# Kernel tuning notes

Hardware: AMD Instinct MI355X
Metric: run time of the kernel (lower is better)

The kernel has to match this reference:

```python
import jax, jax.numpy as jnp
import numpy as np

EPS = 1e-6
NH, NKV, HD = 16, 8, 256
WIN = 1024
NE, TOPK = 32, 4
H, I = 2816, 704


def _rmsnorm(x, w, eps=EPS):
    x32 = x.astype(jnp.float32)
    n = x32 * jax.lax.rsqrt(jnp.mean(x32 * x32, axis=-1, keepdims=True) + eps)
    return n.astype(x.dtype) * w


def _rotate_half(x):
    x1, x2 = jnp.split(x, 2, axis=-1)
    return jnp.concatenate([-x2, x1], axis=-1)


def setup_inputs() -> dict:
    B, S = 1, 512
    key = jax.random.key(0)
    ks = jax.random.split(key, 10)
    sc = 0.02
    hidden_states = jax.random.normal(ks[0], (B, S, H), jnp.float32)
    # rope tables (sliding_attention: theta=10000, full rotary over head_dim)
    pos = np.arange(S, dtype=np.float64)
    inv = 1.0 / (10000.0 ** (np.arange(0, HD, 2, dtype=np.float64) / HD))
    fr = pos[:, None] * inv[None, :]
    emb = np.concatenate([fr, fr], axis=-1)
    cos = jnp.asarray(np.cos(emb)[None], jnp.float32)
    sin = jnp.asarray(np.sin(emb)[None], jnp.float32)
    return dict(
        hidden_states=hidden_states, cos=cos, sin=sin,
        ln_in_w=jnp.ones((H,), jnp.float32),
        ln_post_attn_w=jnp.ones((H,), jnp.float32),
        ln_pre_ffn_w=jnp.ones((H,), jnp.float32),
        ln_post_ffn_w=jnp.ones((H,), jnp.float32),
        q_w=jax.random.normal(ks[1], (NH * HD, H), jnp.float32) * sc,
        k_w=jax.random.normal(ks[2], (NKV * HD, H), jnp.float32) * sc,
        v_w=jax.random.normal(ks[3], (NKV * HD, H), jnp.float32) * sc,
        o_w=jax.random.normal(ks[4], (H, NH * HD), jnp.float32) * sc,
        q_norm_w=jnp.ones((HD,), jnp.float32),
        k_norm_w=jnp.ones((HD,), jnp.float32),
        router_w=jax.random.normal(ks[5], (NE, H), jnp.float32) * sc,
        router_scale=jnp.ones((H,), jnp.float32),
        w_gate=jax.random.normal(ks[6], (NE, I, H), jnp.float32) * sc,
        w_up=jax.random.normal(ks[7], (NE, I, H), jnp.float32) * sc,
        w_down=jax.random.normal(ks[8], (NE, H, I), jnp.float32) * sc,
    )


def reference(hidden_states, cos, sin, ln_in_w, ln_post_attn_w, ln_pre_ffn_w,
              ln_post_ffn_w, q_w, k_w, v_w, o_w, q_norm_w, k_norm_w,
              router_w, router_scale, w_gate, w_up, w_down):
    B, S, _ = hidden_states.shape
    # ---- attention block ----
    res = hidden_states
    h = _rmsnorm(hidden_states, ln_in_w)
    q = (h @ q_w.T).reshape(B, S, NH, HD)
    k = (h @ k_w.T).reshape(B, S, NKV, HD)
    v = (h @ v_w.T).reshape(B, S, NKV, HD)
    q = _rmsnorm(q, q_norm_w)
    k = _rmsnorm(k, k_norm_w)
    v = _rmsnorm(v, jnp.float32(1.0))  # v_norm has no scale
    c, s = cos[:, :, None, :], sin[:, :, None, :]
    q = q * c + _rotate_half(q) * s
    k = k * c + _rotate_half(k) * s
    kr = jnp.repeat(k, NH // NKV, axis=2)  # GQA expand
    vr = jnp.repeat(v, NH // NKV, axis=2)
    scores = jnp.einsum('bqnd,bknd->bnqk', q, kr)  # softmax scale = 1.0
    ii = jnp.arange(S)[:, None]
    jj = jnp.arange(S)[None, :]
    mask = (jj <= ii) & ((ii - jj) < WIN)  # causal + sliding window
    scores = jnp.where(mask, scores, jnp.finfo(scores.dtype).min)
    attn = jax.nn.softmax(scores, axis=-1)
    o = jnp.einsum('bnqk,bknd->bqnd', attn, vr).reshape(B, S, NH * HD)
    h = _rmsnorm(o @ o_w.T, ln_post_attn_w)
    x = res + h
    # ---- MoE block ----
    res = x
    h = _rmsnorm(x, ln_pre_ffn_w)
    t = h.reshape(B * S, H)
    # router: RMSNorm(no scale) * hidden^-0.5 * scale -> linear -> softmax -> topk
    t32 = t.astype(jnp.float32)
    n = (t32 * jax.lax.rsqrt(jnp.mean(t32 * t32, -1, keepdims=True) + EPS)).astype(t.dtype)
    n = n * (H ** -0.5) * router_scale
    probs = jax.nn.softmax(n @ router_w.T, axis=-1)
    topw, topi = jax.lax.top_k(probs, TOPK)
    topw = topw / jnp.sum(topw, axis=-1, keepdims=True)
    T = t.shape[0]
    combine = jnp.zeros((T, NE), t.dtype).at[jnp.arange(T)[:, None], topi].add(topw)
    # gated MLP per expert (dense eval + sparse combine == torch_moe math)
    g = jnp.einsum('th,eih->eti', t, w_gate)
    u = jnp.einsum('th,eih->eti', t, w_up)
    a = jax.nn.gelu(g, approximate=True) * u
    y = jnp.einsum('eti,ehi->eth', a, w_down)  # [E,T,H]
    moe = jnp.einsum('te,eth->th', combine, y).reshape(B, S, H)
    moe = _rmsnorm(moe, ln_post_ffn_w)
    return res + moe
```

## Files before the change

### kernel.cpp

```cpp
#include <hip/hip_runtime.h>

static constexpr int T_S   = 512;
static constexpr int H_DIM = 2816;
static constexpr int HD_   = 256;
static constexpr int N_E   = 32;
static constexpr int TOPK_ = 4;
static constexpr int I_DIM = 704;
static constexpr int Q_N   = 4096;
static constexpr int KV_N  = 2048;
static constexpr int QKV_N = 8192;
static constexpr int NSLOT = 2048;
static constexpr float EPS_ = 1e-6f;

typedef __attribute__((ext_vector_type(4))) float f32x4;
typedef __attribute__((ext_vector_type(8))) short bf16x8;

static __device__ __forceinline__ ushort f2bf(float f) {
  uint u = __float_as_uint(f);
  u += 0x7fffu + ((u >> 16) & 1u);
  return (ushort)(u >> 16);
}
static __device__ __forceinline__ float bf2f(ushort u) {
  return __uint_as_float((uint)u << 16);
}
static __device__ __forceinline__ void split2(float x, ushort& h, ushort& l2) {
  h = f2bf(x);
  l2 = f2bf(x - bf2f(h));
}
static __device__ __forceinline__ void split8(const float4& a, const float4& b,
                                              uint4& H, uint4& L) {
  ushort h0,l0,h1,l1,h2,l2,h3,l3,h4,l4,h5,l5,h6,l6,h7,l7;
  split2(a.x,h0,l0); split2(a.y,h1,l1); split2(a.z,h2,l2); split2(a.w,h3,l3);
  split2(b.x,h4,l4); split2(b.y,h5,l5); split2(b.z,h6,l6); split2(b.w,h7,l7);
  H = (uint4){ (uint)h0|((uint)h1<<16), (uint)h2|((uint)h3<<16),
               (uint)h4|((uint)h5<<16), (uint)h6|((uint)h7<<16) };
  L = (uint4){ (uint)l0|((uint)l1<<16), (uint)l2|((uint)l3<<16),
               (uint)l4|((uint)l5<<16), (uint)l6|((uint)l7<<16) };
}
static __device__ __forceinline__ uint4 pack8(const float4& a, const float4& b) {
  return (uint4){ (uint)f2bf(a.x)|((uint)f2bf(a.y)<<16), (uint)f2bf(a.z)|((uint)f2bf(a.w)<<16),
                  (uint)f2bf(b.x)|((uint)f2bf(b.y)<<16), (uint)f2bf(b.z)|((uint)f2bf(b.w)<<16) };
}

static __device__ __forceinline__ float wave_sum(float v) {
  #pragma unroll
  for (int off = 1; off < 64; off <<= 1) v += __shfl_xor(v, off);
  return v;
}
static __device__ __forceinline__ float block_sum256(float v, float* sm) {
  v = wave_sum(v);
  int w = threadIdx.x >> 6, l = threadIdx.x & 63;
  if (l == 0) sm[w] = v;
  __syncthreads();
  float r = sm[0] + sm[1] + sm[2] + sm[3];
  __syncthreads();
  return r;
}

__global__ __launch_bounds__(256) void k_ln_in(
    const float* __restrict__ hid, const float* __restrict__ w,
    ushort* __restrict__ hhi, ushort* __restrict__ hlo) {
  __shared__ float sm[4];
  int t = blockIdx.x, tid = threadIdx.x;
  const float* row = hid + (size_t)t * H_DIM;
  float x[11]; float s = 0.f;
  #pragma unroll
  for (int j = 0; j < 11; ++j) { x[j] = row[tid + j*256]; s += x[j]*x[j]; }
  s = block_sum256(s, sm);
  float r = rsqrtf(s / (float)H_DIM + EPS_);
  #pragma unroll
  for (int j = 0; j < 11; ++j) {
    int idx = tid + j*256;
    float val = x[j]*r*w[idx];
    ushort h, l2; split2(val, h, l2);
    hhi[(size_t)t*H_DIM + idx] = h;
    hlo[(size_t)t*H_DIM + idx] = l2;
  }
}

__global__ __launch_bounds__(256, 2) void k_gemm_qkv(
    const ushort* __restrict__ Ah, const ushort* __restrict__ Al,
    const float* __restrict__ qw, const float* __restrict__ kw,
    const float* __restrict__ vw, float* __restrict__ Cp) {
  const int K = H_DIM, KS = H_DIM/2, NSs = KS/32;
  __shared__ ushort Ash[4][129][8], Asl[4][129][8];
  __shared__ ushort Bsh[4][65][8],  Bsl[4][65][8];
  int tid = threadIdx.x, w = tid >> 6, l = tid & 63;
  int n0 = blockIdx.x * 64, m0 = blockIdx.y * 128, kz = blockIdx.z;
  int kbase = kz * KS;
  const float* Bp = (n0 < Q_N) ? qw + (size_t)n0*K
                  : (n0 < Q_N+KV_N) ? kw + (size_t)(n0-Q_N)*K
                  : vw + (size_t)(n0-Q_N-KV_N)*K;
  float* C = Cp + (size_t)kz * T_S * QKV_N;
  const int l15 = l & 15, lq = l >> 4;
  const int wm = w >> 1, wn = w & 1;
  const int sar = tid >> 2, sak = tid & 3;
  const ushort* aph = Ah + (size_t)(m0 + sar)*K + kbase + sak*8;
  const ushort* apl = Al + (size_t)(m0 + sar)*K + kbase + sak*8;
  const float*  bp  = Bp + (size_t)sar*K + kbase + sak*8;
  uint4 arh0 = *(const uint4*)(aph);
  uint4 arh1 = *(const uint4*)(aph + (size_t)64*K);
  uint4 arl0 = *(const uint4*)(apl);
  uint4 arl1 = *(const uint4*)(apl + (size_t)64*K);
  float4 brA = *(const float4*)(bp), brB = *(const float4*)(bp + 4);
  f32x4 acc[4][2];
  #pragma unroll
  for (int a = 0; a < 4; ++a)
    #pragma unroll
    for (int b = 0; b < 2; ++b) acc[a][b] = (f32x4){0.f,0.f,0.f,0.f};
  for (int t = 0; t < NSs; ++t) {
    *(uint4*)&Ash[sak][sar][0]    = arh0;
    *(uint4*)&Ash[sak][64+sar][0] = arh1;
    *(uint4*)&Asl[sak][sar][0]    = arl0;
    *(uint4*)&Asl[sak][64+sar][0] = arl1;
    { uint4 H, L; split8(brA, brB, H, L);
      *(uint4*)&Bsh[sak][sar][0] = H;
      *(uint4*)&Bsl[sak][sar][0] = L; }
    __syncthreads();
    if (t + 1 < NSs) {
      int k0 = (t+1)*32;
      arh0 = *(const uint4*)(aph + k0);
      arh1 = *(const uint4*)(aph + (size_t)64*K + k0);
      arl0 = *(const uint4*)(apl + k0);
      arl1 = *(const uint4*)(apl + (size_t)64*K + k0);
      brA = *(const float4*)(bp + k0); brB = *(const float4*)(bp + k0 + 4);
    }
    bf16x8 bh[2], bl[2];
    #pragma unroll
    for (int nf = 0; nf < 2; ++nf) {
      bh[nf] = *(bf16x8*)&Bsh[lq][wn*32 + nf*16 + l15][0];
      bl[nf] = *(bf16x8*)&Bsl[lq][wn*32 + nf*16 + l15][0];
    }
    #pragma unroll
    for (int mf = 0; mf < 4; ++mf) {
// ... 293 lines not shown
    float* __restrict__ topw, int* __restrict__ counts, int* __restrict__ lists) {
  __shared__ float sm[4];
  __shared__ float nrow[H_DIM];
  __shared__ float lg[N_E];
  int t = blockIdx.x, tid = threadIdx.x;
  float ap[11], hd[11]; float s = 0.f;
  #pragma unroll
  for (int j = 0; j < 11; ++j) {
    int idx = tid + j*256;
    ap[j] = aproj0[(size_t)t*H_DIM + idx] + aproj1[(size_t)t*H_DIM + idx];
    hd[j] = hid[(size_t)t*H_DIM + idx];
    s += ap[j]*ap[j];
  }
  s = block_sum256(s, sm);
  float r1 = rsqrtf(s / (float)H_DIM + EPS_);
  float x[11]; float s2 = 0.f;
  #pragma unroll
  for (int j = 0; j < 11; ++j) {
    int idx = tid + j*256;
    x[j] = hd[j] + ap[j]*r1*w_pa[idx];
    s2 += x[j]*x[j];
    xout[(size_t)t*H_DIM + idx] = x[j];
  }
  s2 = block_sum256(s2, sm);
  float r2 = rsqrtf(s2 / (float)H_DIM + EPS_);
  float tv[11]; float s3 = 0.f;
  #pragma unroll
  for (int j = 0; j < 11; ++j) {
    int idx = tid + j*256;
    tv[j] = x[j]*r2*w_pf[idx];
    s3 += tv[j]*tv[j];
    tbf[(size_t)t*H_DIM + idx] = f2bf(tv[j]);
  }
  s3 = block_sum256(s3, sm);
  float r3 = rsqrtf(s3 / (float)H_DIM + EPS_) * rsqrtf((float)H_DIM);
  #pragma unroll
  for (int j = 0; j < 11; ++j) {
    int idx = tid + j*256;
    nrow[idx] = tv[j]*r3*rscale[idx];
  }
  __syncthreads();
  int w = tid >> 6, l = tid & 63;
  #pragma unroll
  for (int ei = 0; ei < 8; ++ei) {
    int e = w*8 + ei;
    const float* rwp = rw + (size_t)e*H_DIM;
    float p = 0.f;
    #pragma unroll 4
    for (int j = 0; j < 44; ++j) p += nrow[l + j*64] * rwp[l + j*64];
    p = wave_sum(p);
    if (l == 0) lg[e] = p;
  }
  __syncthreads();
  if (w == 0) {
    float le = (l < 32) ? lg[l] : -3e38f;
    float m = le;
    #pragma unroll
    for (int off = 1; off < 64; off <<= 1) m = fmaxf(m, __shfl_xor(m, off));
    float p = (l < 32) ? __expf(le - m) : -2.f;
    float v = p; int vi = (l < 32) ? l : 999;
    float selv[TOPK_]; int seli[TOPK_];
    for (int sx = 0; sx < TOPK_; ++sx) {
      float bv = v; int bi = vi;
      #pragma unroll
      for (int off = 1; off < 64; off <<= 1) {
        float ov = __shfl_xor(bv, off); int oi = __shfl_xor(bi, off);
        if (ov > bv || (ov == bv && oi < bi)) { bv = ov; bi = oi; }
      }
      selv[sx] = bv; seli[sx] = bi;
      if (vi == bi) v = -1.f;
    }
    if (l == 0) {
      float wsum = selv[0]+selv[1]+selv[2]+selv[3];
      for (int sx = 0; sx < TOPK_; ++sx) {
        topw[t*TOPK_ + sx] = selv[sx]/wsum;
        int e = seli[sx];
        int pos = atomicAdd(&counts[e], 1);
        lists[e*T_S + pos] = t*TOPK_ + sx;
      }
    }
  }
}

__global__ __launch_bounds__(256, 2) void k_moe_gateup(
    const ushort* __restrict__ tbf, const float* __restrict__ wg,
    const float* __restrict__ wu, const int* __restrict__ counts,
    const int* __restrict__ lists, float* __restrict__ pg, float* __restrict__ pu) {
  const int K = H_DIM, KS = K/4, NS = KS/32;
  __shared__ ushort As[4][129][8];
  __shared__ ushort Bg[4][65][8], Bu[4][65][8];
  __shared__ int lls[128];
  int tid = threadIdx.x, w = tid >> 6, l = tid & 63;
  int e = blockIdx.y, n0 = blockIdx.x * 64;
  int mz = blockIdx.z >> 2, kz = blockIdx.z & 3;
  int m0 = mz * 128, kbase = kz * KS;
  int ne = counts[e];
  if (m0 >= ne) return;
  const int* list = lists + e*T_S;
  if (tid < 128) lls[tid] = (m0 + tid < ne) ? list[m0 + tid] : list[0];
  __syncthreads();
  const int l15 = l & 15, lq = l >> 4;
  const int wm = w >> 1, wn = w & 1;
  const int arow = tid >> 1, aoct = (tid & 1) * 2;
  const ushort* ap = tbf + (size_t)(lls[arow] >> 2)*K + kbase + aoct*8;
  const int bhalf = tid >> 7, brow = (tid & 127) >> 1, boct = (tid & 1) * 2;
  const float* bp = (bhalf ? wu : wg) + ((size_t)e*I_DIM + n0 + brow)*K + kbase + boct*8;
  uint4 a0 = *(const uint4*)(ap), a1 = *(const uint4*)(ap + 8);
  float4 b0 = *(const float4*)(bp),     b1 = *(const float4*)(bp + 4);
  float4 b2 = *(const float4*)(bp + 8), b3 = *(const float4*)(bp + 12);
  f32x4 ag[4][2], au[4][2];
  #pragma unroll
  for (int a = 0; a < 4; ++a)
    #pragma unroll
    for (int b = 0; b < 2; ++b) { ag[a][b] = (f32x4){0.f,0.f,0.f,0.f}; au[a][b] = (f32x4){0.f,0.f,0.f,0.f}; }
  for (int t = 0; t < NS; ++t) {
    *(uint4*)&As[aoct][arow][0]   = a0;
    *(uint4*)&As[aoct+1][arow][0] = a1;
    if (bhalf == 0) {
      *(uint4*)&Bg[boct][brow][0]   = pack8(b0, b1);
      *(uint4*)&Bg[boct+1][brow][0] = pack8(b2, b3);
    } else {
      *(uint4*)&Bu[boct][brow][0]   = pack8(b0, b1);
      *(uint4*)&Bu[boct+1][brow][0] = pack8(b2, b3);
    }
    __syncthreads();
    if (t + 1 < NS) {
      int k0 = (t+1)*32;
      a0 = *(const uint4*)(ap + k0); a1 = *(const uint4*)(ap + k0 + 8);
      b0 = *(const float4*)(bp + k0);     b1 = *(const float4*)(bp + k0 + 4);
      b2 = *(const float4*)(bp + k0 + 8); b3 = *(const float4*)(bp + k0 + 12);
    }
    bf16x8 bgf[2], buf_[2];
    #pragma unroll
    for (int nf = 0; nf < 2; ++nf) {
      bgf[nf]  = *(bf16x8*)&Bg[lq][wn*32 + nf*16 + l15][0];
      buf_[nf] = *(bf16x8*)&Bu[lq][wn*32 + nf*16 + l15][0];
    }
    #pragma unroll
    for (int mf = 0; mf < 4; ++mf) {
      bf16x8 af = *(bf16x8*)&As[lq][wm*64 + mf*16 + l15][0];
      #pragma unroll
      for (int nf = 0; nf < 2; ++nf) {
        ag[mf][nf] = __builtin_amdgcn_mfma_f32_16x16x32_bf16(af, bgf[nf],  ag[mf][nf], 0, 0, 0);
        au[mf][nf] = __builtin_amdgcn_mfma_f32_16x16x32_bf16(af, buf_[nf], au[mf][nf], 0, 0, 0);
      }
    }
    __syncthreads();
  }
  const size_t PSL = (size_t)NSLOT * I_DIM;
  #pragma unroll
  for (int mf = 0; mf < 4; ++mf)
    #pragma unroll
    for (int r = 0; r < 4; ++r) {
      int row = wm*64 + mf*16 + lq*4 + r;
      if (m0 + row < ne) {
        size_t base = (size_t)kz*PSL + (size_t)lls[row]*I_DIM + n0 + wn*32;
        #pragma unroll
        for (int nf = 0; nf < 2; ++nf) {
          pg[base + nf*16 + l15] = ag[mf][nf][r];
          pu[base + nf*16 + l15] = au[mf][nf][r];
        }
      }
    }
}

__global__ __launch_bounds__(192) void k_gelu_reduce(
    const float* __restrict__ pg, const float* __restrict__ pu,
    ushort* __restrict__ abf) {
  int sidx = blockIdx.x, c = threadIdx.x;
  if (c >= 176) return;
  const size_t S4 = (size_t)NSLOT * I_DIM / 4;
  const float4* g = (const float4*)(pg + (size_t)sidx*I_DIM) + c;
  const float4* u = (const float4*)(pu + (size_t)sidx*I_DIM) + c;
  float4 gs = g[0], us = u[0];
  #pragma unroll
  for (int k = 1; k < 4; ++k) {
    float4 gk = g[k*S4], uk = u[k*S4];
    gs.x += gk.x; gs.y += gk.y; gs.z += gk.z; gs.w += gk.w;
    us.x += uk.x; us.y += uk.y; us.z += uk.z; us.w += uk.w;
  }
  float go[4] = {gs.x, gs.y, gs.z, gs.w}, uo[4] = {us.x, us.y, us.z, us.w};
  ushort o[4];
  #pragma unroll
  for (int i = 0; i < 4; ++i) {
    float gg = go[i];
    float th = tanhf(0.7978845608f*(gg + 0.044715f*gg*gg*gg));
    o[i] = f2bf(0.5f*gg*(1.f + th)*uo[i]);
  }
  *(ushort4*)(abf + (size_t)sidx*I_DIM + c*4) = *(ushort4*)o;
}

__global__ __launch_bounds__(256, 2) void k_moe_down(
    const ushort* __restrict__ abf, const float* __restrict__ wd,
    const int* __restrict__ counts, const int* __restrict__ lists,
    float* __restrict__ yp) {
  const int K = I_DIM, KS = K/2, NS = KS/32;
  __shared__ ushort As[4][129][8];
  __shared__ ushort Bs[4][129][8];
  __shared__ int lls[128];
  int tid = threadIdx.x, w = tid >> 6, l = tid & 63;
  int e = blockIdx.y, n0 = blockIdx.x * 128;
  int mz = blockIdx.z >> 1, kz = blockIdx.z & 1;
  int m0 = mz * 128, kbase = kz * KS;
  int ne = counts[e];
  if (m0 >= ne) return;
  const int* list = lists + e*T_S;
  if (tid < 128) lls[tid] = (m0 + tid < ne) ? list[m0 + tid] : 0;
  __syncthreads();
  const int l15 = l & 15, lq = l >> 4;
  const int wm = w >> 1, wn = w & 1;
  const int arow = tid >> 1, aoct = (tid & 1) * 2;
  const ushort* ap = abf + (size_t)lls[arow]*K + kbase + aoct*8;
  const int brow = tid >> 1, boct = (tid & 1) * 2;
  const float* bp = wd + ((size_t)e*H_DIM + n0 + brow)*K + kbase + boct*8;
  uint4 a0 = *(const uint4*)(ap), a1 = *(const uint4*)(ap + 8);
  float4 b0 = *(const float4*)(bp),     b1 = *(const float4*)(bp + 4);
  float4 b2 = *(const float4*)(bp + 8), b3 = *(const float4*)(bp + 12);
  f32x4 acc[4][4];
  #pragma unroll
  for (int a = 0; a < 4; ++a)
    #pragma unroll
    for (int b = 0; b < 4; ++b) acc[a][b] = (f32x4){0.f,0.f,0.f,0.f};
  for (int t = 0; t < NS; ++t) {
    *(uint4*)&As[aoct][arow][0]   = a0;
    *(uint4*)&As[aoct+1][arow][0] = a1;
    *(uint4*)&Bs[boct][brow][0]   = pack8(b0, b1);
    *(uint4*)&Bs[boct+1][brow][0] = pack8(b2, b3);
    __syncthreads();
    if (t + 1 < NS) {
      int k0 = (t+1)*32;
      a0 = *(const uint4*)(ap + k0); a1 = *(const uint4*)(ap + k0 + 8);
      b0 = *(const float4*)(bp + k0);     b1 = *(const float4*)(bp + k0 + 4);
      b2 = *(const float4*)(bp + k0 + 8); b3 = *(const float4*)(bp + k0 + 12);
    }
    bf16x8 bf[4];
    #pragma unroll
    for (int nf = 0; nf < 4; ++nf)
      bf[nf] = *(bf16x8*)&Bs[lq][wn*64 + nf*16 + l15][0];
    #pragma unroll
    for (int mf = 0; mf < 4; ++mf) {
      bf16x8 af = *(bf16x8*)&As[lq][wm*64 + mf*16 + l15][0];
      #pragma unroll
      for (int nf = 0; nf < 4; ++nf)
        acc[mf][nf] = __builtin_amdgcn_mfma_f32_16x16x32_bf16(af, bf[nf], acc[mf][nf], 0, 0, 0);
    }
    __syncthreads();
  }
  const size_t YSL = (size_t)NSLOT * H_DIM;
  #pragma unroll
  for (int mf = 0; mf < 4; ++mf)
    #pragma unroll
    for (int r = 0; r < 4; ++r) {
      int row = wm*64 + mf*16 + lq*4 + r;
      if (m0 + row < ne) {
        size_t base = (size_t)kz*YSL + (size_t)lls[row]*H_DIM + n0 + wn*64;
        #pragma unroll
        for (int nf = 0; nf < 4; ++nf)
          yp[base + nf*16 + l15] = acc[mf][nf][r];
      }
    }
}

__global__ __launch_bounds__(256) void k_combine(
    const float* __restrict__ yp, const float* __restrict__ topw,
    const float* __restrict__ xin, const float* __restrict__ w_pff,
    float* __restrict__ out) {
  __shared__ float sm[4];
  const size_t YSL = (size_t)NSLOT * H_DIM;
  int t = blockIdx.x, tid = threadIdx.x;
  float w0 = topw[t*4+0], w1 = topw[t*4+1], w2 = topw[t*4+2], w3 = topw[t*4+3];
  const float* y0 = yp + (size_t)(t*4+0)*H_DIM;
  const float* y1 = yp + (size_t)(t*4+1)*H_DIM;
  const float* y2 = yp + (size_t)(t*4+2)*H_DIM;
  const float* y3 = yp + (size_t)(t*4+3)*H_DIM;
  float m[11]; float s = 0.f;
  #pragma unroll
  for (int j = 0; j < 11; ++j) {
    int idx = tid + j*256;
    m[j] = w0*(y0[idx]+y0[YSL+idx]) + w1*(y1[idx]+y1[YSL+idx])
         + w2*(y2[idx]+y2[YSL+idx]) + w3*(y3[idx]+y3[YSL+idx]);
    s += m[j]*m[j];
  }
  s = block_sum256(s, sm);
  float r = rsqrtf(s / (float)H_DIM + EPS_);
  #pragma unroll
  for (int j = 0; j < 11; ++j) {
    int idx = tid + j*256;
    out[(size_t)t*H_DIM + idx] = xin[(size_t)t*H_DIM + idx] + m[j]*r*w_pff[idx];
  }
}

extern "C" void kernel_launch(void* const* d_in, const int* in_sizes, int n_in,
                              void* d_out, int out_size, void* d_ws, size_t ws_size,
                              hipStream_t stream) {
  (void)in_sizes; (void)n_in; (void)out_size; (void)ws_size;
  const float* hid   = (const float*)d_in[0];
  const float* cosb  = (const float*)d_in[1];
  const float* sinb  = (const float*)d_in[2];
  const float* w_in  = (const float*)d_in[3];
  const float* w_pa  = (const float*)d_in[4];
  const float* w_pf  = (const float*)d_in[5];
  const float* w_pff = (const float*)d_in[6];
  const float* qw    = (const float*)d_in[7];
  const float* kw    = (const float*)d_in[8];
  const float* vw    = (const float*)d_in[9];
  const float* ow    = (const float*)d_in[10];
  const float* qnw   = (const float*)d_in[11];
  const float* knw   = (const float*)d_in[12];
  const float* rw    = (const float*)d_in[13];
  const float* rsc   = (const float*)d_in[14];
  const float* wg    = (const float*)d_in[15];
  const float* wu    = (const float*)d_in[16];
  const float* wd    = (const float*)d_in[17];

  char* ws = (char*)d_ws;
  size_t off = 0;
  auto alloc = [&](size_t sz) { size_t o = off; off += (sz + 255) & ~(size_t)255; return o; };
  size_t oR1  = alloc(46137344);
  size_t ohh  = alloc((size_t)T_S*H_DIM*2);
  size_t ohl  = alloc((size_t)T_S*H_DIM*2);
  size_t oqh  = alloc((size_t)T_S*QKV_N*2);
  size_t oql  = alloc((size_t)T_S*QKV_N*2);
  size_t ovh  = alloc((size_t)8*HD_*T_S*2);
  size_t ovl  = alloc((size_t)8*HD_*T_S*2);
  size_t ox   = alloc((size_t)T_S*H_DIM*4);
  size_t otbf = alloc((size_t)T_S*H_DIM*2);
  size_t otw  = alloc((size_t)T_S*TOPK_*4);
  size_t ocnt = alloc((size_t)N_E*4);
  size_t olst = alloc((size_t)N_E*T_S*4);

  const size_t APRJ_SLICE = (size_t)T_S * H_DIM * 4;

  float*  qkvf0 = (float*)(ws + oR1);
  float*  qkvf1 = (float*)(ws + oR1 + 16777216);
  ushort* o_hi  = (ushort*)(ws + oR1);
  ushort* o_lo  = (ushort*)(ws + oR1 + 4194304);
  float*  aprj0 = (float*)(ws + oR1 + 8388608);
  float*  aprj1 = (float*)(ws + oR1 + 8388608 + APRJ_SLICE);
  float*  pg    = (float*)(ws + oR1);
  float*  pu    = (float*)(ws + oR1 + 23068672);
  float*  yp    = (float*)(ws + oR1);
  ushort* abf   = (ushort*)(ws + ohh);

  k_ln_in<<<dim3(T_S), dim3(256), 0, stream>>>(hid, w_in, (ushort*)(ws+ohh), (ushort*)(ws+ohl));
  k_gemm_qkv<<<dim3(128, 4, 2), dim3(256), 0, stream>>>((ushort*)(ws+ohh), (ushort*)(ws+ohl),
                                                        qw, kw, vw, qkvf0);
  k_norm_rope<<<dim3(T_S*32), dim3(64), 0, stream>>>(qkvf0, qkvf1, cosb, sinb, qnw, knw,
                                                     (ushort*)(ws+oqh), (ushort*)(ws+oql),
                                                     (ushort*)(ws+ovh), (ushort*)(ws+ovl));
  k_attn<<<dim3(8, 16), dim3(256), 0, stream>>>((ushort*)(ws+oqh), (ushort*)(ws+oql),
                                                (ushort*)(ws+ovh), (ushort*)(ws+ovl), o_hi, o_lo);
  k_gemm_oproj<<<dim3(44, 4, 2), dim3(256), 0, stream>>>(o_hi, o_lo, ow, aprj0);
  k_zero_counts<<<dim3(1), dim3(64), 0, stream>>>((int*)(ws+ocnt));
  k_fuse_router<<<dim3(T_S), dim3(256), 0, stream>>>(hid, aprj0, aprj1, w_pa, w_pf, rsc, rw,
                                                     (float*)(ws+ox), (ushort*)(ws+otbf),
                                                     (float*)(ws+otw), (int*)(ws+ocnt), (int*)(ws+olst));
  k_moe_gateup<<<dim3(11, N_E, 16), dim3(256), 0, stream>>>((ushort*)(ws+otbf), wg, wu,
                                                            (int*)(ws+ocnt), (int*)(ws+olst), pg, pu);
  k_gelu_reduce<<<dim3(NSLOT), dim3(192), 0, stream>>>(pg, pu, abf);
  k_moe_down<<<dim3(22, N_E, 8), dim3(256), 0, stream>>>(abf, wd,
                                                         (int*)(ws+ocnt), (int*)(ws+olst), yp);
  k_combine<<<dim3(T_S), dim3(256), 0, stream>>>(yp, (float*)(ws+otw), (float*)(ws+ox),
                                                 w_pff, (float*)d_out);
}
```

Before: 610.9 us.

## Restructure MoE GEMMs to stream weights directly and loop over token tiles

Both MoE expert GEMMs now stage the whole K-slice of gathered activations for a 64-token tile in shared memory. Each wave streams its fp32 weight columns straight from global into registers, with no shared-memory staging for B. Each block loops over all of its expert's token tiles, so weights are read once per (expert, column, k-split) instead of once per 128-token tile. Gate/up now uses an 8-way K split with bf16 partial outputs to cut partial-buffer traffic, at some cost in reduction precision, and down uses a 2-way split. The risks are lower parallelism when experts get many tokens, exposed global-load latency without a prefetch pipeline, and bf16 rounding of the partial sums.

```diff
diff --git a/kernel.cpp b/kernel.cpp
--- a/kernel.cpp
+++ b/kernel.cpp
@@ -509,183 +509,160 @@
   }
 }
 
-__global__ __launch_bounds__(256, 2) void k_moe_gateup(
+__global__ __launch_bounds__(256, 3) void k_moe_gateup(
     const ushort* __restrict__ tbf, const float* __restrict__ wg,
     const float* __restrict__ wu, const int* __restrict__ counts,
-    const int* __restrict__ lists, float* __restrict__ pg, float* __restrict__ pu) {
-  const int K = H_DIM, KS = K/4, NS = KS/32;
-  __shared__ ushort As[4][129][8];
-  __shared__ ushort Bg[4][65][8], Bu[4][65][8];
-  __shared__ int lls[128];
+    const int* __restrict__ lists, ushort* __restrict__ pgb, ushort* __restrict__ pub) {
+  const int K = H_DIM, KS = K/8, NSTEP = KS/32;
+  __shared__ ushort As[44][67][8];
+  __shared__ int lls[64];
   int tid = threadIdx.x, w = tid >> 6, l = tid & 63;
-  int e = blockIdx.y, n0 = blockIdx.x * 64;
-  int mz = blockIdx.z >> 2, kz = blockIdx.z & 3;
-  int m0 = mz * 128, kbase = kz * KS;
+  int e = blockIdx.y, n0 = blockIdx.x * 64, kz = blockIdx.z;
+  int kbase = kz * KS;
   int ne = counts[e];
-  if (m0 >= ne) return;
   const int* list = lists + e*T_S;
-  if (tid < 128) lls[tid] = (m0 + tid < ne) ? list[m0 + tid] : list[0];
-  __syncthreads();
   const int l15 = l & 15, lq = l >> 4;
-  const int wm = w >> 1, wn = w & 1;
-  const int arow = tid >> 1, aoct = (tid & 1) * 2;
-  const ushort* ap = tbf + (size_t)(lls[arow] >> 2)*K + kbase + aoct*8;
-  const int bhalf = tid >> 7, brow = (tid & 127) >> 1, boct = (tid & 1) * 2;
-  const float* bp = (bhalf ? wu : wg) + ((size_t)e*I_DIM + n0 + brow)*K + kbase + boct*8;
-  uint4 a0 = *(const uint4*)(ap), a1 = *(const uint4*)(ap + 8);
-  float4 b0 = *(const float4*)(bp),     b1 = *(const float4*)(bp + 4);
-  float4 b2 = *(const float4*)(bp + 8), b3 = *(const float4*)(bp + 12);
-  f32x4 ag[4][2], au[4][2];
-  #pragma unroll
-  for (int a = 0; a < 4; ++a)
-    #pragma unroll
-    for (int b = 0; b < 2; ++b) { ag[a][b] = (f32x4){0.f,0.f,0.f,0.f}; au[a][b] = (f32x4){0.f,0.f,0.f,0.f}; }
-  for (int t = 0; t < NS; ++t) {
-    *(uint4*)&As[aoct][arow][0]   = a0;
-    *(uint4*)&As[aoct+1][arow][0] = a1;
-    if (bhalf == 0) {
-      *(uint4*)&Bg[boct][brow][0]   = pack8(b0, b1);
-      *(uint4*)&Bg[boct+1][brow][0] = pack8(b2, b3);
-    } else {
-      *(uint4*)&Bu[boct][brow][0]   = pack8(b0, b1);
-      *(uint4*)&Bu[boct+1][brow][0] = pack8(b2, b3);
-    }
-    __syncthreads();
-    if (t + 1 < NS) {
-      int k0 = (t+1)*32;
-      a0 = *(const uint4*)(ap + k0); a1 = *(const uint4*)(ap + k0 + 8);
-      b0 = *(const float4*)(bp + k0);     b1 = *(const float4*)(bp + k0 + 4);
-      b2 = *(const float4*)(bp + k0 + 8); b3 = *(const float4*)(bp + k0 + 12);
-    }
-    bf16x8 bgf[2], buf_[2];
-    #pragma unroll
-    for (int nf = 0; nf < 2; ++nf) {
-      bgf[nf]  = *(bf16x8*)&Bg[lq][wn*32 + nf*16 + l15][0];
-      buf_[nf] = *(bf16x8*)&Bu[lq][wn*32 + nf*16 + l15][0];
-    }
-    #pragma unroll
-    for (int mf = 0; mf < 4; ++mf) {
-      bf16x8 af = *(bf16x8*)&As[lq][wm*64 + mf*16 + l15][0];
-      #pragma unroll
-      for (int nf = 0; nf < 2; ++nf) {
-        ag[mf][nf] = __builtin_amdgcn_mfma_f32_16x16x32_bf16(af, bgf[nf],  ag[mf][nf], 0, 0, 0);
-        au[mf][nf] = __builtin_amdgcn_mfma_f32_16x16x32_bf16(af, buf_[nf], au[mf][nf], 0, 0, 0);
-      }
-    }
-    __syncthreads();
-  }
+  const float* Bmat = (w < 2) ? wg : wu;
+  ushort* Pout = (w < 2) ? pgb : pub;
+  const int col0 = n0 + (w & 1) * 32;
+  const float* bptr0 = Bmat + ((size_t)e*I_DIM + col0 + l15)*K + kbase + lq*8;
+  const float* bptr1 = Bmat + ((size_t)e*I_DIM + col0 + 16 + l15)*K + kbase + lq*8;
   const size_t PSL = (size_t)NSLOT * I_DIM;
-  #pragma unroll
-  for (int mf = 0; mf < 4; ++mf)
-    #pragma unroll
-    for (int r = 0; r < 4; ++r) {
-      int row = wm*64 + mf*16 + lq*4 + r;
-      if (m0 + row < ne) {
-        size_t base = (size_t)kz*PSL + (size_t)lls[row]*I_DIM + n0 + wn*32;
-        #pragma unroll
-        for (int nf = 0; nf < 2; ++nf) {
-          pg[base + nf*16 + l15] = ag[mf][nf][r];
-          pu[base + nf*16 + l15] = au[mf][nf][r];
+  for (int m0 = 0; m0 < ne; m0 += 64) {
+    if (m0 > 0) __syncthreads();
+    if (tid < 64) lls[tid] = (m0 + tid < ne) ? list[m0 + tid] : list[0];
+    __syncthreads();
+    #pragma unroll
+    for (int p = 0; p < 11; ++p) {
+      int c = p*256 + tid;
+      int row = c / 44, oct = c - row*44;
+      const ushort* src = tbf + (size_t)(lls[row] >> 2)*K + kbase + oct*8;
+      *(uint4*)&As[oct][row][0] = *(const uint4*)src;
+    }
+    __syncthreads();
+    f32x4 acc[4][2];
+    #pragma unroll
+    for (int a = 0; a < 4; ++a)
+      #pragma unroll
+      for (int b = 0; b < 2; ++b) acc[a][b] = (f32x4){0.f,0.f,0.f,0.f};
+    for (int s = 0; s < NSTEP; ++s) {
+      int k0 = s*32;
+      float4 f00 = *(const float4*)(bptr0 + k0);
+      float4 f01 = *(const float4*)(bptr0 + k0 + 4);
+      float4 f10 = *(const float4*)(bptr1 + k0);
+      float4 f11 = *(const float4*)(bptr1 + k0 + 4);
+      uint4 B0 = pack8(f00, f01), B1 = pack8(f10, f11);
+      bf16x8 b0 = *(bf16x8*)&B0, b1 = *(bf16x8*)&B1;
+      int ko = s*4 + lq;
+      #pragma unroll
+      for (int mf = 0; mf < 4; ++mf) {
+        bf16x8 af = *(bf16x8*)&As[ko][mf*16 + l15][0];
+        acc[mf][0] = __builtin_amdgcn_mfma_f32_16x16x32_bf16(af, b0, acc[mf][0], 0, 0, 0);
+        acc[mf][1] = __builtin_amdgcn_mfma_f32_16x16x32_bf16(af, b1, acc[mf][1], 0, 0, 0);
+      }
+    }
+    #pragma unroll
+    for (int mf = 0; mf < 4; ++mf)
+      #pragma unroll
+      for (int r = 0; r < 4; ++r) {
+        int row = mf*16 + lq*4 + r;
+        if (m0 + row < ne) {
+          size_t base = (size_t)kz*PSL + (size_t)lls[row]*I_DIM + col0;
+          Pout[base + l15]      = f2bf(acc[mf][0][r]);
+          Pout[base + 16 + l15] = f2bf(acc[mf][1][r]);
         }
       }
-    }
+  }
 }
 
 __global__ __launch_bounds__(192) void k_gelu_reduce(
-    const float* __restrict__ pg, const float* __restrict__ pu,
+    const ushort* __restrict__ pgb, const ushort* __restrict__ pub,
     ushort* __restrict__ abf) {
   int sidx = blockIdx.x, c = threadIdx.x;
   if (c >= 176) return;
-  const size_t S4 = (size_t)NSLOT * I_DIM / 4;
-  const float4* g = (const float4*)(pg + (size_t)sidx*I_DIM) + c;
-  const float4* u = (const float4*)(pu + (size_t)sidx*I_DIM) + c;
-  float4 gs = g[0], us = u[0];
-  #pragma unroll
-  for (int k = 1; k < 4; ++k) {
-    float4 gk = g[k*S4], uk = u[k*S4];
-    gs.x += gk.x; gs.y += gk.y; gs.z += gk.z; gs.w += gk.w;
-    us.x += uk.x; us.y += uk.y; us.z += uk.z; us.w += uk.w;
-  }
-  float go[4] = {gs.x, gs.y, gs.z, gs.w}, uo[4] = {us.x, us.y, us.z, us.w};
+  const size_t S8 = (size_t)NSLOT * I_DIM;
+  const ushort* g = pgb + (size_t)sidx*I_DIM + c*4;
+  const ushort* u = pub + (size_t)sidx*I_DIM + c*4;
+  float gs[4] = {0.f,0.f,0.f,0.f}, us[4] = {0.f,0.f,0.f,0.f};
+  #pragma unroll
+  for (int k = 0; k < 8; ++k) {
+    ushort4 gv = *(const ushort4*)(g + k*S8);
+    ushort4 uv = *(const ushort4*)(u + k*S8);
+    gs[0] += bf2f(gv.x); gs[1] += bf2f(gv.y); gs[2] += bf2f(gv.z); gs[3] += bf2f(gv.w);
+    us[0] += bf2f(uv.x); us[1] += bf2f(uv.y); us[2] += bf2f(uv.z); us[3] += bf2f(uv.w);
+  }
   ushort o[4];
   #pragma unroll
   for (int i = 0; i < 4; ++i) {
-    float gg = go[i];
+    float gg = gs[i];
     float th = tanhf(0.7978845608f*(gg + 0.044715f*gg*gg*gg));
-    o[i] = f2bf(0.5f*gg*(1.f + th)*uo[i]);
+    o[i] = f2bf(0.5f*gg*(1.f + th)*us[i]);
   }
   *(ushort4*)(abf + (size_t)sidx*I_DIM + c*4) = *(ushort4*)o;
 }
 
-__global__ __launch_bounds__(256, 2) void k_moe_down(
+__global__ __launch_bounds__(256, 3) void k_moe_down(
     const ushort* __restrict__ abf, const float* __restrict__ wd,
     const int* __restrict__ counts, const int* __restrict__ lists,
     float* __restrict__ yp) {
-  const int K = I_DIM, KS = K/2, NS = KS/32;
-  __shared__ ushort As[4][129][8];
-  __shared__ ushort Bs[4][129][8];
-  __shared__ int lls[128];
+  const int K = I_DIM, KS = K/2, NSTEP = KS/32;
+  __shared__ ushort As[44][67][8];
+  __shared__ int lls[64];
   int tid = threadIdx.x, w = tid >> 6, l = tid & 63;
-  int e = blockIdx.y, n0 = blockIdx.x * 128;
-  int mz = blockIdx.z >> 1, kz = blockIdx.z & 1;
-  int m0 = mz * 128, kbase = kz * KS;
+  int e = blockIdx.y, n0 = blockIdx.x * 128, kz = blockIdx.z;
+  int kbase = kz * KS;
   int ne = counts[e];
-  if (m0 >= ne) return;
   const int* list = lists + e*T_S;
-  if (tid < 128) lls[tid] = (m0 + tid < ne) ? list[m0 + tid] : 0;
-  __syncthreads();
   const int l15 = l & 15, lq = l >> 4;
-  const int wm = w >> 1, wn = w & 1;
-  const int arow = tid >> 1, aoct = (tid & 1) * 2;
-  const ushort* ap = abf + (size_t)lls[arow]*K + kbase + aoct*8;
-  const int brow = tid >> 1, boct = (tid & 1) * 2;
-  const float* bp = wd + ((size_t)e*H_DIM + n0 + brow)*K + kbase + boct*8;
-  uint4 a0 = *(const uint4*)(ap), a1 = *(const uint4*)(ap + 8);
-  float4 b0 = *(const float4*)(bp),     b1 = *(const float4*)(bp + 4);
-  float4 b2 = *(const float4*)(bp + 8), b3 = *(const float4*)(bp + 12);
-  f32x4 acc[4][4];
-  #pragma unroll
-  for (int a = 0; a < 4; ++a)
-    #pragma unroll
-    for (int b = 0; b < 4; ++b) acc[a][b] = (f32x4){0.f,0.f,0.f,0.f};
-  for (int t = 0; t < NS; ++t) {
-    *(uint4*)&As[aoct][arow][0]   = a0;
-    *(uint4*)&As[aoct+1][arow][0] = a1;
-    *(uint4*)&Bs[boct][brow][0]   = pack8(b0, b1);
-    *(uint4*)&Bs[boct+1][brow][0] = pack8(b2, b3);
-    __syncthreads();
-    if (t + 1 < NS) {
-      int k0 = (t+1)*32;
-      a0 = *(const uint4*)(ap + k0); a1 = *(const uint4*)(ap + k0 + 8);
-      b0 = *(const float4*)(bp + k0);     b1 = *(const float4*)(bp + k0 + 4);
-      b2 = *(const float4*)(bp + k0 + 8); b3 = *(const float4*)(bp + k0 + 12);
-    }
-    bf16x8 bf[4];
-    #pragma unroll
-    for (int nf = 0; nf < 4; ++nf)
-      bf[nf] = *(bf16x8*)&Bs[lq][wn*64 + nf*16 + l15][0];
-    #pragma unroll
-    for (int mf = 0; mf < 4; ++mf) {
-      bf16x8 af = *(bf16x8*)&As[lq][wm*64 + mf*16 + l15][0];
-      #pragma unroll
-      for (int nf = 0; nf < 4; ++nf)
-        acc[mf][nf] = __builtin_amdgcn_mfma_f32_16x16x32_bf16(af, bf[nf], acc[mf][nf], 0, 0, 0);
-    }
-    __syncthreads();
-  }
+  const int col0 = n0 + w * 32;
+  const float* bptr0 = wd + ((size_t)e*H_DIM + col0 + l15)*K + kbase + lq*8;
+  const float* bptr1 = wd + ((size_t)e*H_DIM + col0 + 16 + l15)*K + kbase + lq*8;
   const size_t YSL = (size_t)NSLOT * H_DIM;
-  #pragma unroll
-  for (int mf = 0; mf < 4; ++mf)
-    #pragma unroll
-    for (int r = 0; r < 4; ++r) {
-      int row = wm*64 + mf*16 + lq*4 + r;
-      if (m0 + row < ne) {
-        size_t base = (size_t)kz*YSL + (size_t)lls[row]*H_DIM + n0 + wn*64;
-        #pragma unroll
-        for (int nf = 0; nf < 4; ++nf)
-          yp[base + nf*16 + l15] = acc[mf][nf][r];
-      }
-    }
+  for (int m0 = 0; m0 < ne; m0 += 64) {
+    if (m0 > 0) __syncthreads();
+    if (tid < 64) lls[tid] = (m0 + tid < ne) ? list[m0 + tid] : 0;
+    __syncthreads();
+    #pragma unroll
+    for (int p = 0; p < 11; ++p) {
+      int c = p*256 + tid;
+      int row = c / 44, oct = c - row*44;
+      const ushort* src = abf + (size_t)lls[row]*K + kbase + oct*8;
+      *(uint4*)&As[oct][row][0] = *(const uint4*)src;
+    }
+    __syncthreads();
+    f32x4 acc[4][2];
+    #pragma unroll
+    for (int a = 0; a < 4; ++a)
+      #pragma unroll
+      for (int b = 0; b < 2; ++b) acc[a][b] = (f32x4){0.f,0.f,0.f,0.f};
+    for (int s = 0; s < NSTEP; ++s) {
+      int k0 = s*32;
+      float4 f00 = *(const float4*)(bptr0 + k0);
+      float4 f01 = *(const float4*)(bptr0 + k0 + 4);
+      float4 f10 = *(const float4*)(bptr1 + k0);
+      float4 f11 = *(const float4*)(bptr1 + k0 + 4);
+      uint4 B0 = pack8(f00, f01), B1 = pack8(f10, f11);
+      bf16x8 b0 = *(bf16x8*)&B0, b1 = *(bf16x8*)&B1;
+      int ko = s*4 + lq;
+      #pragma unroll
+      for (int mf = 0; mf < 4; ++mf) {
+        bf16x8 af = *(bf16x8*)&As[ko][mf*16 + l15][0];
+        acc[mf][0] = __builtin_amdgcn_mfma_f32_16x16x32_bf16(af, b0, acc[mf][0], 0, 0, 0);
+        acc[mf][1] = __builtin_amdgcn_mfma_f32_16x16x32_bf16(af, b1, acc[mf][1], 0, 0, 0);
+      }
+    }
+    #pragma unroll
+    for (int mf = 0; mf < 4; ++mf)
+      #pragma unroll
+      for (int r = 0; r < 4; ++r) {
+        int row = mf*16 + lq*4 + r;
+        if (m0 + row < ne) {
+          size_t base = (size_t)kz*YSL + (size_t)lls[row]*H_DIM + col0;
+          yp[base + l15]      = acc[mf][0][r];
+          yp[base + 16 + l15] = acc[mf][1][r];
+        }
+      }
+  }
 }
 
 __global__ __launch_bounds__(256) void k_combine(
@@ -764,8 +741,8 @@
   ushort* o_lo  = (ushort*)(ws + oR1 + 4194304);
   float*  aprj0 = (float*)(ws + oR1 + 8388608);
   float*  aprj1 = (float*)(ws + oR1 + 8388608 + APRJ_SLICE);
-  float*  pg    = (float*)(ws + oR1);
-  float*  pu    = (float*)(ws + oR1 + 23068672);
+  ushort* pgb   = (ushort*)(ws + oR1);
+  ushort* pub   = (ushort*)(ws + oR1 + 23068672);
   float*  yp    = (float*)(ws + oR1);
   ushort* abf   = (ushort*)(ws + ohh);
 
@@ -782,10 +759,10 @@
   k_fuse_router<<<dim3(T_S), dim3(256), 0, stream>>>(hid, aprj0, aprj1, w_pa, w_pf, rsc, rw,
                                                      (float*)(ws+ox), (ushort*)(ws+otbf),
                                                      (float*)(ws+otw), (int*)(ws+ocnt), (int*)(ws+olst));
-  k_moe_gateup<<<dim3(11, N_E, 16), dim3(256), 0, stream>>>((ushort*)(ws+otbf), wg, wu,
-                                                            (int*)(ws+ocnt), (int*)(ws+olst), pg, pu);
-  k_gelu_reduce<<<dim3(NSLOT), dim3(192), 0, stream>>>(pg, pu, abf);
-  k_moe_down<<<dim3(22, N_E, 8), dim3(256), 0, stream>>>(abf, wd,
+  k_moe_gateup<<<dim3(11, N_E, 8), dim3(256), 0, stream>>>((ushort*)(ws+otbf), wg, wu,
+                                                           (int*)(ws+ocnt), (int*)(ws+olst), pgb, pub);
+  k_gelu_reduce<<<dim3(NSLOT), dim3(192), 0, stream>>>(pgb, pub, abf);
+  k_moe_down<<<dim3(22, N_E, 2), dim3(256), 0, stream>>>(abf, wd,
                                                          (int*)(ws+ocnt), (int*)(ws+olst), yp);
   k_combine<<<dim3(T_S), dim3(256), 0, stream>>>(yp, (float*)(ws+otw), (float*)(ws+ox),
                                                  w_pff, (float*)d_out);
```

Result: slower. 656.4 us (+7.4%).

## Stage MoE GEMM tiles via direct global-to-LDS loads and raise occupancy

Applied to the files above, without the earlier changes.

The MoE gate/up and down GEMM kernels now copy A and fp32 B tiles straight from global memory into LDS with global_load_lds, replacing the register-staged loads, and convert B to bf16 when reading it out of LDS. Launch bounds go from 2 to 4 blocks per SM, since fewer registers are held for prefetched tiles. The register double-buffered prefetch is gone, so loads are no longer overlapped with MFMA work except through the extra resident blocks. The fp32 B tile doubles its LDS footprint, and the padded layouts were dropped, which may add bank conflicts.

```diff
diff --git a/kernel.cpp b/kernel.cpp
--- a/kernel.cpp
+++ b/kernel.cpp
@@ -41,6 +41,14 @@
   return (uint4){ (uint)f2bf(a.x)|((uint)f2bf(a.y)<<16), (uint)f2bf(a.z)|((uint)f2bf(a.w)<<16),
                   (uint)f2bf(b.x)|((uint)f2bf(b.y)<<16), (uint)f2bf(b.z)|((uint)f2bf(b.w)<<16) };
 }
+static __device__ __forceinline__ ushort4 pack4(const float4& a) {
+  return (ushort4){ f2bf(a.x), f2bf(a.y), f2bf(a.z), f2bf(a.w) };
+}
+static __device__ __forceinline__ void gld_lds16(const void* g, void* l) {
+  __builtin_amdgcn_global_load_lds(
+      (const __attribute__((address_space(1))) uint*)g,
+      (__attribute__((address_space(3))) uint*)l, 16, 0, 0);
+}
 
 static __device__ __forceinline__ float wave_sum(float v) {
   #pragma unroll
@@ -48,8 +56,8 @@
   return v;
 }
 static __device__ __forceinline__ float block_sum256(float v, float* sm) {
+  int w = threadIdx.x >> 6, l = threadIdx.x & 63;
   v = wave_sum(v);
-  int w = threadIdx.x >> 6, l = threadIdx.x & 63;
   if (l == 0) sm[w] = v;
   __syncthreads();
   float r = sm[0] + sm[1] + sm[2] + sm[3];
@@ -509,13 +517,14 @@
   }
 }
 
-__global__ __launch_bounds__(256, 2) void k_moe_gateup(
+__global__ __launch_bounds__(256, 4) void k_moe_gateup(
     const ushort* __restrict__ tbf, const float* __restrict__ wg,
     const float* __restrict__ wu, const int* __restrict__ counts,
     const int* __restrict__ lists, float* __restrict__ pg, float* __restrict__ pu) {
   const int K = H_DIM, KS = K/4, NS = KS/32;
-  __shared__ ushort As[4][129][8];
-  __shared__ ushort Bg[4][65][8], Bu[4][65][8];
+  __shared__ ushort As[4][128][8];
+  __shared__ float  Bg[8][64][4];
+  __shared__ float  Bu[8][64][4];
   __shared__ int lls[128];
   int tid = threadIdx.x, w = tid >> 6, l = tid & 63;
   int e = blockIdx.y, n0 = blockIdx.x * 64;
@@ -528,40 +537,45 @@
   __syncthreads();
   const int l15 = l & 15, lq = l >> 4;
   const int wm = w >> 1, wn = w & 1;
-  const int arow = tid >> 1, aoct = (tid & 1) * 2;
-  const ushort* ap = tbf + (size_t)(lls[arow] >> 2)*K + kbase + aoct*8;
-  const int bhalf = tid >> 7, brow = (tid & 127) >> 1, boct = (tid & 1) * 2;
-  const float* bp = (bhalf ? wu : wg) + ((size_t)e*I_DIM + n0 + brow)*K + kbase + boct*8;
-  uint4 a0 = *(const uint4*)(ap), a1 = *(const uint4*)(ap + 8);
-  float4 b0 = *(const float4*)(bp),     b1 = *(const float4*)(bp + 4);
-  float4 b2 = *(const float4*)(bp + 8), b3 = *(const float4*)(bp + 12);
+  int cA0 = (w*2+0)*64 + l, cA1 = (w*2+1)*64 + l;
+  const ushort* gA0 = tbf + (size_t)(lls[cA0 & 127] >> 2)*K + kbase + (cA0 >> 7)*8;
+  const ushort* gA1 = tbf + (size_t)(lls[cA1 & 127] >> 2)*K + kbase + (cA1 >> 7)*8;
+  const float* gG0 = wg + ((size_t)e*I_DIM + n0 + (cA0 & 63))*K + kbase + (cA0 >> 6)*4;
+  const float* gG1 = wg + ((size_t)e*I_DIM + n0 + (cA1 & 63))*K + kbase + (cA1 >> 6)*4;
+  const float* gU0 = wu + ((size_t)e*I_DIM + n0 + (cA0 & 63))*K + kbase + (cA0 >> 6)*4;
+  const float* gU1 = wu + ((size_t)e*I_DIM + n0 + (cA1 & 63))*K + kbase + (cA1 >> 6)*4;
+  char* lA0 = (char*)As + (w*2+0)*1024;
+  char* lA1 = (char*)As + (w*2+1)*1024;
+  char* lG0 = (char*)Bg + (w*2+0)*1024;
+  char* lG1 = (char*)Bg + (w*2+1)*1024;
+  char* lU0 = (char*)Bu + (w*2+0)*1024;
+  char* lU1 = (char*)Bu + (w*2+1)*1024;
   f32x4 ag[4][2], au[4][2];
   #pragma unroll
   for (int a = 0; a < 4; ++a)
     #pragma unroll
     for (int b = 0; b < 2; ++b) { ag[a][b] = (f32x4){0.f,0.f,0.f,0.f}; au[a][b] = (f32x4){0.f,0.f,0.f,0.f}; }
   for (int t = 0; t < NS; ++t) {
-    *(uint4*)&As[aoct][arow][0]   = a0;
-    *(uint4*)&As[aoct+1][arow][0] = a1;
-    if (bhalf == 0) {
-      *(uint4*)&Bg[boct][brow][0]   = pack8(b0, b1);
-      *(uint4*)&Bg[boct+1][brow][0] = pack8(b2, b3);
-    } else {
-      *(uint4*)&Bu[boct][brow][0]   = pack8(b0, b1);
-      *(uint4*)&Bu[boct+1][brow][0] = pack8(b2, b3);
-    }
-    __syncthreads();
-    if (t + 1 < NS) {
-      int k0 = (t+1)*32;
-      a0 = *(const uint4*)(ap + k0); a1 = *(const uint4*)(ap + k0 + 8);
-      b0 = *(const float4*)(bp + k0);     b1 = *(const float4*)(bp + k0 + 4);
-      b2 = *(const float4*)(bp + k0 + 8); b3 = *(const float4*)(bp + k0 + 12);
-    }
+    int ko = t*32;
+    __syncthreads();
+    gld_lds16(gA0 + ko, lA0);
+    gld_lds16(gA1 + ko, lA1);
+    gld_lds16(gG0 + ko, lG0);
+    gld_lds16(gG1 + ko, lG1);
+    gld_lds16(gU0 + ko, lU0);
+    gld_lds16(gU1 + ko, lU1);
+    __syncthreads();
     bf16x8 bgf[2], buf_[2];
     #pragma unroll
     for (int nf = 0; nf < 2; ++nf) {
-      bgf[nf]  = *(bf16x8*)&Bg[lq][wn*32 + nf*16 + l15][0];
-      buf_[nf] = *(bf16x8*)&Bu[lq][wn*32 + nf*16 + l15][0];
+      int rowb = wn*32 + nf*16 + l15;
+      float4 g0 = *(const float4*)&Bg[lq*2+0][rowb][0];
+      float4 g1 = *(const float4*)&Bg[lq*2+1][rowb][0];
+      float4 u0 = *(const float4*)&Bu[lq*2+0][rowb][0];
+      float4 u1 = *(const float4*)&Bu[lq*2+1][rowb][0];
+      uint4 G = pack8(g0, g1), U = pack8(u0, u1);
+      bgf[nf] = *(bf16x8*)&G;
+      buf_[nf] = *(bf16x8*)&U;
     }
     #pragma unroll
     for (int mf = 0; mf < 4; ++mf) {
@@ -572,7 +586,6 @@
         au[mf][nf] = __builtin_amdgcn_mfma_f32_16x16x32_bf16(af, buf_[nf], au[mf][nf], 0, 0, 0);
       }
     }
-    __syncthreads();
   }
   const size_t PSL = (size_t)NSLOT * I_DIM;
   #pragma unroll
@@ -617,13 +630,13 @@
   *(ushort4*)(abf + (size_t)sidx*I_DIM + c*4) = *(ushort4*)o;
 }
 
-__global__ __launch_bounds__(256, 2) void k_moe_down(
+__global__ __launch_bounds__(256, 4) void k_moe_down(
     const ushort* __restrict__ abf, const float* __restrict__ wd,
     const int* __restrict__ counts, const int* __restrict__ lists,
     float* __restrict__ yp) {
   const int K = I_DIM, KS = K/2, NS = KS/32;
-  __shared__ ushort As[4][129][8];
-  __shared__ ushort Bs[4][129][8];
+  __shared__ ushort As[4][128][8];
+  __shared__ float  Bs[8][128][4];
   __shared__ int lls[128];
   int tid = threadIdx.x, w = tid >> 6, l = tid & 63;
   int e = blockIdx.y, n0 = blockIdx.x * 128;
@@ -636,34 +649,44 @@
   __syncthreads();
   const int l15 = l & 15, lq = l >> 4;
   const int wm = w >> 1, wn = w & 1;
-  const int arow = tid >> 1, aoct = (tid & 1) * 2;
-  const ushort* ap = abf + (size_t)lls[arow]*K + kbase + aoct*8;
-  const int brow = tid >> 1, boct = (tid & 1) * 2;
-  const float* bp = wd + ((size_t)e*H_DIM + n0 + brow)*K + kbase + boct*8;
-  uint4 a0 = *(const uint4*)(ap), a1 = *(const uint4*)(ap + 8);
-  float4 b0 = *(const float4*)(bp),     b1 = *(const float4*)(bp + 4);
-  float4 b2 = *(const float4*)(bp + 8), b3 = *(const float4*)(bp + 12);
+  int cA0 = (w*2+0)*64 + l, cA1 = (w*2+1)*64 + l;
+  const ushort* gA0 = abf + (size_t)lls[cA0 & 127]*K + kbase + (cA0 >> 7)*8;
+  const ushort* gA1 = abf + (size_t)lls[cA1 & 127]*K + kbase + (cA1 >> 7)*8;
+  int cB0 = (w*4+0)*64 + l, cB1 = (w*4+1)*64 + l, cB2 = (w*4+2)*64 + l, cB3 = (w*4+3)*64 + l;
+  const float* gB0 = wd + ((size_t)e*H_DIM + n0 + (cB0 & 127))*K + kbase + (cB0 >> 7)*4;
+  const float* gB1 = wd + ((size_t)e*H_DIM + n0 + (cB1 & 127))*K + kbase + (cB1 >> 7)*4;
+  const float* gB2 = wd + ((size_t)e*H_DIM + n0 + (cB2 & 127))*K + kbase + (cB2 >> 7)*4;
+  const float* gB3 = wd + ((size_t)e*H_DIM + n0 + (cB3 & 127))*K + kbase + (cB3 >> 7)*4;
+  char* lA0 = (char*)As + (w*2+0)*1024;
+  char* lA1 = (char*)As + (w*2+1)*1024;
+  char* lB0 = (char*)Bs + (w*4+0)*1024;
+  char* lB1 = (char*)Bs + (w*4+1)*1024;
+  char* lB2 = (char*)Bs + (w*4+2)*1024;
+  char* lB3 = (char*)Bs + (w*4+3)*1024;
   f32x4 acc[4][4];
   #pragma unroll
   for (int a = 0; a < 4; ++a)
     #pragma unroll
     for (int b = 0; b < 4; ++b) acc[a][b] = (f32x4){0.f,0.f,0.f,0.f};
   for (int t = 0; t < NS; ++t) {
-    *(uint4*)&As[aoct][arow][0]   = a0;
-    *(uint4*)&As[aoct+1][arow][0] = a1;
-    *(uint4*)&Bs[boct][brow][0]   = pack8(b0, b1);
-    *(uint4*)&Bs[boct+1][brow][0] = pack8(b2, b3);
-    __syncthreads();
-    if (t + 1 < NS) {
-      int k0 = (t+1)*32;
-      a0 = *(const uint4*)(ap + k0); a1 = *(const uint4*)(ap + k0 + 8);
-      b0 = *(const float4*)(bp + k0);     b1 = *(const float4*)(bp + k0 + 4);
-      b2 = *(const float4*)(bp + k0 + 8); b3 = *(const float4*)(bp + k0 + 12);
-    }
+    int ko = t*32;
+    __syncthreads();
+    gld_lds16(gA0 + ko, lA0);
+    gld_lds16(gA1 + ko, lA1);
+    gld_lds16(gB0 + ko, lB0);
+    gld_lds16(gB1 + ko, lB1);
+    gld_lds16(gB2 + ko, lB2);
+    gld_lds16(gB3 + ko, lB3);
+    __syncthreads();
     bf16x8 bf[4];
     #pragma unroll
-    for (int nf = 0; nf < 4; ++nf)
-      bf[nf] = *(bf16x8*)&Bs[lq][wn*64 + nf*16 + l15][0];
+    for (int nf = 0; nf < 4; ++nf) {
+      int rowb = wn*64 + nf*16 + l15;
+      float4 f0 = *(const float4*)&Bs[lq*2+0][rowb][0];
+      float4 f1 = *(const float4*)&Bs[lq*2+1][rowb][0];
+      uint4 P = pack8(f0, f1);
+      bf[nf] = *(bf16x8*)&P;
+    }
     #pragma unroll
     for (int mf = 0; mf < 4; ++mf) {
       bf16x8 af = *(bf16x8*)&As[lq][wm*64 + mf*16 + l15][0];
@@ -671,7 +694,6 @@
       for (int nf = 0; nf < 4; ++nf)
         acc[mf][nf] = __builtin_amdgcn_mfma_f32_16x16x32_bf16(af, bf[nf], acc[mf][nf], 0, 0, 0);
     }
-    __syncthreads();
   }
   const size_t YSL = (size_t)NSLOT * H_DIM;
   #pragma unroll
```

After: 646.2 us. +5.8%, slower.
